# Optimization experiments

Hardware: AMD Instinct MI355X
Metric: run time of the kernel (lower is better)

Reference implementation:

```python
import jax, jax.numpy as jnp
import numpy as np

B, N, E, DIN, DH = 32, 2000, 64000, 128, 128


def setup_inputs() -> dict:
    key = jax.random.key(0)
    ks = jax.random.split(key, 8)
    gene_emb = jax.random.normal(ks[0], (B, N, DIN), dtype=jnp.float32)
    edge_src = jax.random.randint(ks[1], (E,), 0, N, dtype=jnp.int32)
    edge_dst = jax.random.randint(ks[2], (E,), 0, N, dtype=jnp.int32)
    s1 = 1.0 / np.sqrt(DIN)
    s2 = 1.0 / np.sqrt(DH)
    W1 = jax.random.normal(ks[3], (DIN, DH), dtype=jnp.float32) * s1
    b1 = jnp.zeros((DH,), dtype=jnp.float32)
    W2 = jax.random.normal(ks[4], (DH, DH), dtype=jnp.float32) * s2
    b2 = jnp.zeros((DH,), dtype=jnp.float32)
    return {"gene_emb": gene_emb, "edge_src": edge_src, "edge_dst": edge_dst,
            "W1": W1, "b1": b1, "W2": W2, "b2": b2, "pathway_idx": 0}


def _gcn_conv(x, src, dst, norm_e, self_norm, W, b):
    # x: [B, N, Din] -> [B, N, Dout]; PyG GCNConv: linear first, then normalized aggregation
    h = jnp.einsum('bnd,de->bne', x, W)
    msgs = h[:, src, :] * norm_e[None, :, None]          # [B, E, Dout] gather
    agg = jax.vmap(lambda m: jax.ops.segment_sum(m, dst, num_segments=h.shape[1]))(msgs)
    # self-loop contribution (A+I): norm = dinv[i]^2
    return agg + h * self_norm[None, :, None] + b


def reference(gene_emb, edge_src, edge_dst, W1, b1, W2, b2, pathway_idx):
    n = gene_emb.shape[1]
    # symmetric GCN normalization with self loops: deg[i] = in_degree + 1
    deg = jnp.zeros((n,), dtype=gene_emb.dtype).at[edge_dst].add(1.0) + 1.0
    dinv = jax.lax.rsqrt(deg)
    norm_e = dinv[edge_src] * dinv[edge_dst]
    self_norm = dinv * dinv
    x = jax.nn.relu(_gcn_conv(gene_emb, edge_src, edge_dst, norm_e, self_norm, W1, b1))
    x = _gcn_conv(x, edge_src, edge_dst, norm_e, self_norm, W2, b2)
    # global_mean_pool over each graph copy (all graphs have n nodes)
    return jnp.mean(x, axis=1)  # [B, DH]
```

## Files before the change

### kernel.cpp

```cpp
#include <hip/hip_runtime.h>

namespace {
constexpr int NB = 32;
constexpr int NN = 2000;
constexpr int NE = 64000;
constexpr int ND = 128;
constexpr int TR = 32;
constexpr int NCHUNK = (NN + TR - 1) / TR;
constexpr int NXCD = 8;
constexpr int BPB = 2;
constexpr int PAIRS = NB / (NXCD * BPB);
constexpr int GRID_FUSED = NXCD * PAIRS * NCHUNK;
constexpr int SL = 80;
constexpr int ECAP = 1536;

constexpr int CVT_BLOCKS  = 8000;
constexpr int EDGE_BLOCKS = 250;

constexpr size_t OFF_CNT  = 0;
constexpr size_t OFF_WSUM = OFF_CNT + 2048 * 4;
constexpr size_t OFF_SLOT = OFF_WSUM + 2048 * 4;
constexpr size_t OFF_XBF  = OFF_SLOT + (size_t)NN * SL * 4;
constexpr size_t OFF_YP   = OFF_XBF + (size_t)NB * NN * ND * 2;
constexpr size_t MEMSET_BYTES = 2048 * 4 * 2;

__device__ __forceinline__ ushort f32_to_bf16(float f) {
    uint u = __float_as_uint(f);
    u += 0x7fffu + ((u >> 16) & 1u);
    return (ushort)(u >> 16);
}
}

__global__ void k_fill(const float* __restrict__ X, ushort* __restrict__ xbf,
                       const int* __restrict__ src, const int* __restrict__ dst,
                       int* __restrict__ cnt, int* __restrict__ slot) {
    const int blk = blockIdx.x;
    if (blk < CVT_BLOCKS) {
        int i = blk * 256 + threadIdx.x;
        float4 v = ((const float4*)X)[i];
        ushort4 o;
        o.x = f32_to_bf16(v.x);
        o.y = f32_to_bf16(v.y);
        o.z = f32_to_bf16(v.z);
        o.w = f32_to_bf16(v.w);
        ((ushort4*)xbf)[i] = o;
    } else {
        int e = (blk - CVT_BLOCKS) * 256 + threadIdx.x;
        int s = src[e], d = dst[e];
        int p = atomicAdd(&cnt[d], 1);
        if (p < SL) slot[d * SL + p] = s;
    }
}

__global__ void k_wsum(const int* __restrict__ src, const int* __restrict__ dst,
                       const int* __restrict__ cnt, float* __restrict__ wsum) {
    int e = blockIdx.x * 256 + threadIdx.x;
    if (e < NE) {
        int s = src[e], d = dst[e];
        float w = rsqrtf((float)(cnt[s] + 1)) * rsqrtf((float)(cnt[d] + 1));
        atomicAdd(&wsum[s], w);
    }
}

__global__ __launch_bounds__(256, 3) void k_fused(const ushort* __restrict__ xbf,
                                                  const int* __restrict__ cnt,
                                                  const int* __restrict__ slot,
                                                  const float* __restrict__ wsum,
                                                  const float* __restrict__ W1,
                                                  const float* __restrict__ b1,
                                                  float* __restrict__ ypart) {
    __shared__ float4 As4[2][32 * 33];
    __shared__ int2   sEdge[ECAP];
    __shared__ int    sCnt[32];
    __shared__ int    sBase[33];
    __shared__ float  sDinv[32];
    __shared__ float  yred[2][128];
    const int tid = threadIdx.x;

    const int L     = blockIdx.x;
    const int xcd   = L & (NXCD - 1);
    const int sl    = L >> 3;
    const int pair  = sl / NCHUNK;
    const int chunk = sl % NCHUNK;
    const int b0    = xcd * (BPB * PAIRS) + pair * BPB;
    const int n0    = chunk * TR;

    if (tid < 32) {
        int n = n0 + tid;
        int cr = (n < NN) ? cnt[n] : 0;
        sCnt[tid]  = min(cr, SL);
        sDinv[tid] = rsqrtf((float)(cr + 1));
    }
    if (tid < 128) { yred[0][tid] = 0.f; yred[1][tid] = 0.f; }
    __syncthreads();
    if (tid == 0) {
        int s = 0;
        for (int j = 0; j < 32; j++) { sBase[j] = s; s += sCnt[j]; }
        sBase[32] = s;
    }
    __syncthreads();
    const bool staged = (sBase[32] <= ECAP);

    const int wv = tid >> 6, ln = tid & 63;
    if (staged) {
        for (int ii = 0; ii < 8; ii++) {
            int j = wv * 8 + ii;
            int c = sCnt[j];
            float dd = sDinv[j];
            const int* sp = &slot[(size_t)(n0 + j) * SL];
            for (int base = 0; base < c; base += 64) {
                if (base + ln < c) {
                    int sidx = sp[base + ln];
                    float w = rsqrtf((float)(cnt[sidx] + 1)) * dd;
                    sEdge[sBase[j] + base + ln] = make_int2(sidx, __float_as_int(w));
                }
            }
        }
    }
    __syncthreads();

    const uint* __restrict__ Xu0 = (const uint*)(xbf + (size_t)b0 * NN * ND);
    const uint* __restrict__ Xu1 = (const uint*)(xbf + (size_t)(b0 + 1) * NN * ND);
    float2* A0 = (float2*)As4[0];
    float2* A1 = (float2*)As4[1];
    #pragma unroll 1
    for (int ii = 0; ii < 8; ii++) {
        const int j = wv * 8 + ii;
        const int n = n0 + j;
        float2 a0 = make_float2(0.f, 0.f), a1 = a0, a0b = a0, a1b = a0;
        if (n < NN) {
            float sn = sDinv[j]; sn *= sn;
            uint u0 = Xu0[n * 64 + ln], u1 = Xu1[n * 64 + ln];
            a0.x = sn * __uint_as_float(u0 << 16);
            a0.y = sn * __uint_as_float(u0 & 0xffff0000u);
            a1.x = sn * __uint_as_float(u1 << 16);
            a1.y = sn * __uint_as_float(u1 & 0xffff0000u);
            const int c = sCnt[j];
            if (staged) {
                const int e0 = sBase[j], e1 = e0 + c;
                int e = e0;
                for (; e + 8 <= e1; e += 8) {
                    int sidx[8]; float w[8]; uint q0[8], q1[8];
                    #pragma unroll
                    for (int q = 0; q < 8; q++) {
                        int2 ed = sEdge[e + q];
                        sidx[q] = ed.x; w[q] = __int_as_float(ed.y);
                    }
                    #pragma unroll
                    for (int q = 0; q < 8; q++) {
                        q0[q] = Xu0[sidx[q] * 64 + ln];
                        q1[q] = Xu1[sidx[q] * 64 + ln];
                    }
                    #pragma unroll
                    for (int q = 0; q < 8; q++) {
                        float x0l = __uint_as_float(q0[q] << 16);
                        float x0h = __uint_as_float(q0[q] & 0xffff0000u);
                        float x1l = __uint_as_float(q1[q] << 16);
                        float x1h = __uint_as_float(q1[q] & 0xffff0000u);
                        if (q & 1) {
                            a0b.x = fmaf(w[q], x0l, a0b.x);
                            a0b.y = fmaf(w[q], x0h, a0b.y);
                            a1b.x = fmaf(w[q], x1l, a1b.x);
                            a1b.y = fmaf(w[q], x1h, a1b.y);
                        } else {
                            a0.x = fmaf(w[q], x0l, a0.x);
                            a0.y = fmaf(w[q], x0h, a0.y);
                            a1.x = fmaf(w[q], x1l, a1.x);
                            a1.y = fmaf(w[q], x1h, a1.y);
                        }
                    }
                }
                for (; e < e1; e++) {
                    int2 ed = sEdge[e];
                    float w = __int_as_float(ed.y);
                    uint u0e = Xu0[ed.x * 64 + ln], u1e = Xu1[ed.x * 64 + ln];
                    a0.x = fmaf(w, __uint_as_float(u0e << 16), a0.x);
                    a0.y = fmaf(w, __uint_as_float(u0e & 0xffff0000u), a0.y);
                    a1.x = fmaf(w, __uint_as_float(u1e << 16), a1.x);
                    a1.y = fmaf(w, __uint_as_float(u1e & 0xffff0000u), a1.y);
                }
            } else {
                const int* sp = &slot[(size_t)n * SL];
                float dd = sDinv[j];
                for (int e = 0; e < c; e++) {
                    int sidx = sp[e];
                    float w = rsqrtf((float)(cnt[sidx] + 1)) * dd;
                    uint u0e = Xu0[sidx * 64 + ln], u1e = Xu1[sidx * 64 + ln];
                    a0.x = fmaf(w, __uint_as_float(u0e << 16), a0.x);
                    a0.y = fmaf(w, __uint_as_float(u0e & 0xffff0000u), a0.y);
                    a1.x = fmaf(w, __uint_as_float(u1e << 16), a1.x);
                    a1.y = fmaf(w, __uint_as_float(u1e & 0xffff0000u), a1.y);
                }
            }
            a0.x += a0b.x; a0.y += a0b.y;
            a1.x += a1b.x; a1.y += a1b.y;
        }
        A0[j * 66 + ln] = a0;
        A1[j * 66 + ln] = a1;
    }
    __syncthreads();

    const int c4 = tid & 31, rg = tid >> 5;
    float4 acc0[4], acc1[4];
    #pragma unroll
    for (int i = 0; i < 4; i++) {
        acc0[i] = make_float4(0.f, 0.f, 0.f, 0.f);
        acc1[i] = make_float4(0.f, 0.f, 0.f, 0.f);
    }
    const float4* __restrict__ W4 = (const float4*)W1 + c4;
    #pragma unroll 2
    for (int k4 = 0; k4 < 32; k4++) {
        float4 w0 = W4[(4 * k4 + 0) * 32];
        float4 w1 = W4[(4 * k4 + 1) * 32];
        float4 w2 = W4[(4 * k4 + 2) * 32];
        float4 w3 = W4[(4 * k4 + 3) * 32];
        #pragma unroll
        for (int i = 0; i < 4; i++) {
            float4 a = As4[0][(rg * 4 + i) * 33 + k4];
            acc0[i].x = fmaf(a.x, w0.x, acc0[i].x); acc0[i].x = fmaf(a.y, w1.x, acc0[i].x);
            acc0[i].x = fmaf(a.z, w2.x, acc0[i].x); acc0[i].x = fmaf(a.w, w3.x, acc0[i].x);
            acc0[i].y = fmaf(a.x, w0.y, acc0[i].y); acc0[i].y = fmaf(a.y, w1.y, acc0[i].y);
            acc0[i].y = fmaf(a.z, w2.y, acc0[i].y); acc0[i].y = fmaf(a.w, w3.y, acc0[i].y);
            acc0[i].z = fmaf(a.x, w0.z, acc0[i].z); acc0[i].z = fmaf(a.y, w1.z, acc0[i].z);
            acc0[i].z = fmaf(a.z, w2.z, acc0[i].z); acc0[i].z = fmaf(a.w, w3.z, acc0[i].z);
            acc0[i].w = fmaf(a.x, w0.w, acc0[i].w); acc0[i].w = fmaf(a.y, w1.w, acc0[i].w);
            acc0[i].w = fmaf(a.z, w2.w, acc0[i].w); acc0[i].w = fmaf(a.w, w3.w, acc0[i].w);
            float4 b = As4[1][(rg * 4 + i) * 33 + k4];
            acc1[i].x = fmaf(b.x, w0.x, acc1[i].x); acc1[i].x = fmaf(b.y, w1.x, acc1[i].x);
            acc1[i].x = fmaf(b.z, w2.x, acc1[i].x); acc1[i].x = fmaf(b.w, w3.x, acc1[i].x);
            acc1[i].y = fmaf(b.x, w0.y, acc1[i].y); acc1[i].y = fmaf(b.y, w1.y, acc1[i].y);
            acc1[i].y = fmaf(b.z, w2.y, acc1[i].y); acc1[i].y = fmaf(b.w, w3.y, acc1[i].y);
            acc1[i].z = fmaf(b.x, w0.z, acc1[i].z); acc1[i].z = fmaf(b.y, w1.z, acc1[i].z);
            acc1[i].z = fmaf(b.z, w2.z, acc1[i].z); acc1[i].z = fmaf(b.w, w3.z, acc1[i].z);
            acc1[i].w = fmaf(b.x, w0.w, acc1[i].w); acc1[i].w = fmaf(b.y, w1.w, acc1[i].w);
            acc1[i].w = fmaf(b.z, w2.w, acc1[i].w); acc1[i].w = fmaf(b.w, w3.w, acc1[i].w);
        }
    }

    float wn[4];
    #pragma unroll
    for (int i = 0; i < 4; i++) {
        int j = rg * 4 + i, n = n0 + j;
        float sd = sDinv[j];
        wn[i] = (n < NN) ? (wsum[n] + sd * sd) : 0.f;
    }
    float4 bias = ((const float4*)b1)[c4];
    float4 ya0 = make_float4(0.f, 0.f, 0.f, 0.f);
    float4 ya1 = ya0;
    #pragma unroll
    for (int i = 0; i < 4; i++) {
        ya0.x = fmaf(wn[i], fmaxf(acc0[i].x + bias.x, 0.f), ya0.x);
        ya0.y = fmaf(wn[i], fmaxf(acc0[i].y + bias.y, 0.f), ya0.y);
        ya0.z = fmaf(wn[i], fmaxf(acc0[i].z + bias.z, 0.f), ya0.z);
        ya0.w = fmaf(wn[i], fmaxf(acc0[i].w + bias.w, 0.f), ya0.w);
        ya1.x = fmaf(wn[i], fmaxf(acc1[i].x + bias.x, 0.f), ya1.x);
        ya1.y = fmaf(wn[i], fmaxf(acc1[i].y + bias.y, 0.f), ya1.y);
        ya1.z = fmaf(wn[i], fmaxf(acc1[i].z + bias.z, 0.f), ya1.z);
        ya1.w = fmaf(wn[i], fmaxf(acc1[i].w + bias.w, 0.f), ya1.w);
    }
    atomicAdd(&yred[0][4 * c4 + 0], ya0.x); atomicAdd(&yred[0][4 * c4 + 1], ya0.y);
    atomicAdd(&yred[0][4 * c4 + 2], ya0.z); atomicAdd(&yred[0][4 * c4 + 3], ya0.w);
    atomicAdd(&yred[1][4 * c4 + 0], ya1.x); atomicAdd(&yred[1][4 * c4 + 1], ya1.y);
    atomicAdd(&yred[1][4 * c4 + 2], ya1.z); atomicAdd(&yred[1][4 * c4 + 3], ya1.w);
    __syncthreads();
    if (tid < 128)
        ypart[((size_t)b0 * NCHUNK + chunk) * ND + tid] = yred[0][tid];
    else
        ypart[((size_t)(b0 + 1) * NCHUNK + chunk) * ND + (tid - 128)] = yred[1][tid - 128];
}

__global__ __launch_bounds__(128) void k_out(const float* __restrict__ ypart,
                                             const float* __restrict__ W2,
                                             const float* __restrict__ b2,
                                             float* __restrict__ out) {
    __shared__ float ys[128];
    const int b = blockIdx.x;
    const int d = threadIdx.x;
    float s = 0.f;
    for (int c = 0; c < NCHUNK; c++)
        s += ypart[((size_t)b * NCHUNK + c) * ND + d];
    ys[d] = s * (1.f / (float)NN);
    __syncthreads();
    float acc = b2[d];
    #pragma unroll 8
    for (int k = 0; k < 128; k++)
        acc = fmaf(ys[k], W2[k * ND + d], acc);
    out[b * ND + d] = acc;
}

extern "C" void kernel_launch(void* const* d_in, const int* in_sizes, int n_in,
                              void* d_out, int out_size, void* d_ws, size_t ws_size,
                              hipStream_t stream) {
    (void)in_sizes; (void)n_in; (void)out_size; (void)ws_size;
    const float* X   = (const float*)d_in[0];
    const int*   src = (const int*)d_in[1];
    const int*   dst = (const int*)d_in[2];
    const float* W1  = (const float*)d_in[3];
    const float* b1  = (const float*)d_in[4];
    const float* W2  = (const float*)d_in[5];
    const float* b2  = (const float*)d_in[6];
    float* out = (float*)d_out;

    char* ws = (char*)d_ws;
    int*    cnt   = (int*)   (ws + OFF_CNT);
    float*  wsum  = (float*) (ws + OFF_WSUM);
    int*    slot  = (int*)   (ws + OFF_SLOT);
    ushort* xbf   = (ushort*)(ws + OFF_XBF);
    float*  ypart = (float*) (ws + OFF_YP);

    (void)hipMemsetAsync(ws, 0, MEMSET_BYTES, stream);
    k_fill<<<CVT_BLOCKS + EDGE_BLOCKS, 256, 0, stream>>>(X, xbf, src, dst, cnt, slot);
    k_wsum<<<EDGE_BLOCKS, 256, 0, stream>>>(src, dst, cnt, wsum);
    k_fused<<<GRID_FUSED, 256, 0, stream>>>(xbf, cnt, slot, wsum, W1, b1, ypart);
    k_out<<<NB, 128, 0, stream>>>(ypart, W2, b2, out);
}
```

Measured before the change: 195.8 us.

## Use bf16 MFMA for the first-layer transform with prepacked W1 fragments

Replaces the fp32 scalar-FMA 32x128x128 GEMM in the fused kernel with bf16 MFMA 16x16x32 instructions. The aggregated rows are stored to LDS as packed bf16, and W1 is pre-converted into per-lane MFMA fragment layout in an extra section of the fill kernel. Shared memory shrinks and launch bounds rise to 4 blocks per CU, aiming to cut ALU time and raise occupancy. The cost is extra precision loss from rounding the aggregated activations and weights to bf16.

```diff
diff --git a/kernel.cpp b/kernel.cpp
--- a/kernel.cpp
+++ b/kernel.cpp
@@ -15,23 +15,32 @@
 constexpr int ECAP = 1536;
 
 constexpr int CVT_BLOCKS  = 8000;
+constexpr int W_BLOCKS    = 8;
 constexpr int EDGE_BLOCKS = 250;
 
 constexpr size_t OFF_CNT  = 0;
 constexpr size_t OFF_WSUM = OFF_CNT + 2048 * 4;
 constexpr size_t OFF_SLOT = OFF_WSUM + 2048 * 4;
-constexpr size_t OFF_XBF  = OFF_SLOT + (size_t)NN * SL * 4;
+constexpr size_t OFF_WF   = OFF_SLOT + (size_t)NN * SL * 4;
+constexpr size_t OFF_XBF  = OFF_WF + 32768;
 constexpr size_t OFF_YP   = OFF_XBF + (size_t)NB * NN * ND * 2;
 constexpr size_t MEMSET_BYTES = 2048 * 4 * 2;
+
+typedef __attribute__((ext_vector_type(8))) short bf16x8;
+typedef __attribute__((ext_vector_type(4))) float f32x4;
 
 __device__ __forceinline__ ushort f32_to_bf16(float f) {
     uint u = __float_as_uint(f);
     u += 0x7fffu + ((u >> 16) & 1u);
     return (ushort)(u >> 16);
 }
+__device__ __forceinline__ uint pack_bf16x2(float lo, float hi) {
+    return (uint)f32_to_bf16(lo) | ((uint)f32_to_bf16(hi) << 16);
+}
 }
 
 __global__ void k_fill(const float* __restrict__ X, ushort* __restrict__ xbf,
+                       const float* __restrict__ W1, uint* __restrict__ wf,
                        const int* __restrict__ src, const int* __restrict__ dst,
                        int* __restrict__ cnt, int* __restrict__ slot) {
     const int blk = blockIdx.x;
@@ -44,8 +53,20 @@
         o.z = f32_to_bf16(v.z);
         o.w = f32_to_bf16(v.w);
         ((ushort4*)xbf)[i] = o;
+    } else if (blk < CVT_BLOCKS + W_BLOCKS) {
+        int g = (blk - CVT_BLOCKS) * 256 + threadIdx.x;
+        int lane = g & 63, f = g >> 6;
+        int nt = f >> 2, kc = f & 3;
+        int col = nt * 16 + (lane & 15);
+        int k0  = kc * 32 + (lane >> 4) * 8;
+        uint4 o;
+        o.x = pack_bf16x2(W1[(k0 + 0) * ND + col], W1[(k0 + 1) * ND + col]);
+        o.y = pack_bf16x2(W1[(k0 + 2) * ND + col], W1[(k0 + 3) * ND + col]);
+        o.z = pack_bf16x2(W1[(k0 + 4) * ND + col], W1[(k0 + 5) * ND + col]);
+        o.w = pack_bf16x2(W1[(k0 + 6) * ND + col], W1[(k0 + 7) * ND + col]);
+        ((uint4*)wf)[g] = o;
     } else {
-        int e = (blk - CVT_BLOCKS) * 256 + threadIdx.x;
+        int e = (blk - CVT_BLOCKS - W_BLOCKS) * 256 + threadIdx.x;
         int s = src[e], d = dst[e];
         int p = atomicAdd(&cnt[d], 1);
         if (p < SL) slot[d * SL + p] = s;
@@ -62,19 +83,20 @@
     }
 }
 
-__global__ __launch_bounds__(256, 3) void k_fused(const ushort* __restrict__ xbf,
+__global__ __launch_bounds__(256, 4) void k_fused(const ushort* __restrict__ xbf,
                                                   const int* __restrict__ cnt,
                                                   const int* __restrict__ slot,
                                                   const float* __restrict__ wsum,
-                                                  const float* __restrict__ W1,
+                                                  const uint* __restrict__ wfrag,
                                                   const float* __restrict__ b1,
                                                   float* __restrict__ ypart) {
-    __shared__ float4 As4[2][32 * 33];
-    __shared__ int2   sEdge[ECAP];
-    __shared__ int    sCnt[32];
-    __shared__ int    sBase[33];
-    __shared__ float  sDinv[32];
-    __shared__ float  yred[2][128];
+    __shared__ uint  AsU[2][32 * 68];
+    __shared__ int2  sEdge[ECAP];
+    __shared__ int   sCnt[32];
+    __shared__ int   sBase[33];
+    __shared__ float sDinv[32];
+    __shared__ float sWn[32];
+    __shared__ float yred[2][128];
     const int tid = threadIdx.x;
 
     const int L     = blockIdx.x;
@@ -88,8 +110,10 @@
     if (tid < 32) {
         int n = n0 + tid;
         int cr = (n < NN) ? cnt[n] : 0;
+        float d = rsqrtf((float)(cr + 1));
         sCnt[tid]  = min(cr, SL);
-        sDinv[tid] = rsqrtf((float)(cr + 1));
+        sDinv[tid] = d;
+        sWn[tid]   = (n < NN) ? (wsum[n] + d * d) : 0.f;
     }
     if (tid < 128) { yred[0][tid] = 0.f; yred[1][tid] = 0.f; }
     __syncthreads();
@@ -121,8 +145,6 @@
 
     const uint* __restrict__ Xu0 = (const uint*)(xbf + (size_t)b0 * NN * ND);
     const uint* __restrict__ Xu1 = (const uint*)(xbf + (size_t)(b0 + 1) * NN * ND);
-    float2* A0 = (float2*)As4[0];
-    float2* A1 = (float2*)As4[1];
     #pragma unroll 1
     for (int ii = 0; ii < 8; ii++) {
         const int j = wv * 8 + ii;
@@ -195,73 +217,67 @@
             a0.x += a0b.x; a0.y += a0b.y;
             a1.x += a1b.x; a1.y += a1b.y;
         }
-        A0[j * 66 + ln] = a0;
-        A1[j * 66 + ln] = a1;
-    }
-    __syncthreads();
-
-    const int c4 = tid & 31, rg = tid >> 5;
-    float4 acc0[4], acc1[4];
+        AsU[0][j * 68 + ln] = pack_bf16x2(a0.x, a0.y);
+        AsU[1][j * 68 + ln] = pack_bf16x2(a1.x, a1.y);
+    }
+    __syncthreads();
+
+    const int lane15 = ln & 15, quad = ln >> 4;
+    f32x4 zero4 = {0.f, 0.f, 0.f, 0.f};
+    f32x4 acc[2][2][2];
     #pragma unroll
-    for (int i = 0; i < 4; i++) {
-        acc0[i] = make_float4(0.f, 0.f, 0.f, 0.f);
-        acc1[i] = make_float4(0.f, 0.f, 0.f, 0.f);
-    }
-    const float4* __restrict__ W4 = (const float4*)W1 + c4;
-    #pragma unroll 2
-    for (int k4 = 0; k4 < 32; k4++) {
-        float4 w0 = W4[(4 * k4 + 0) * 32];
-        float4 w1 = W4[(4 * k4 + 1) * 32];
-        float4 w2 = W4[(4 * k4 + 2) * 32];
-        float4 w3 = W4[(4 * k4 + 3) * 32];
+    for (int b = 0; b < 2; b++)
         #pragma unroll
-        for (int i = 0; i < 4; i++) {
-            float4 a = As4[0][(rg * 4 + i) * 33 + k4];
-            acc0[i].x = fmaf(a.x, w0.x, acc0[i].x); acc0[i].x = fmaf(a.y, w1.x, acc0[i].x);
-            acc0[i].x = fmaf(a.z, w2.x, acc0[i].x); acc0[i].x = fmaf(a.w, w3.x, acc0[i].x);
-            acc0[i].y = fmaf(a.x, w0.y, acc0[i].y); acc0[i].y = fmaf(a.y, w1.y, acc0[i].y);
-            acc0[i].y = fmaf(a.z, w2.y, acc0[i].y); acc0[i].y = fmaf(a.w, w3.y, acc0[i].y);
-            acc0[i].z = fmaf(a.x, w0.z, acc0[i].z); acc0[i].z = fmaf(a.y, w1.z, acc0[i].z);
-            acc0[i].z = fmaf(a.z, w2.z, acc0[i].z); acc0[i].z = fmaf(a.w, w3.z, acc0[i].z);
-            acc0[i].w = fmaf(a.x, w0.w, acc0[i].w); acc0[i].w = fmaf(a.y, w1.w, acc0[i].w);
-            acc0[i].w = fmaf(a.z, w2.w, acc0[i].w); acc0[i].w = fmaf(a.w, w3.w, acc0[i].w);
-            float4 b = As4[1][(rg * 4 + i) * 33 + k4];
-            acc1[i].x = fmaf(b.x, w0.x, acc1[i].x); acc1[i].x = fmaf(b.y, w1.x, acc1[i].x);
-            acc1[i].x = fmaf(b.z, w2.x, acc1[i].x); acc1[i].x = fmaf(b.w, w3.x, acc1[i].x);
-            acc1[i].y = fmaf(b.x, w0.y, acc1[i].y); acc1[i].y = fmaf(b.y, w1.y, acc1[i].y);
-            acc1[i].y = fmaf(b.z, w2.y, acc1[i].y); acc1[i].y = fmaf(b.w, w3.y, acc1[i].y);
-            acc1[i].z = fmaf(b.x, w0.z, acc1[i].z); acc1[i].z = fmaf(b.y, w1.z, acc1[i].z);
-            acc1[i].z = fmaf(b.z, w2.z, acc1[i].z); acc1[i].z = fmaf(b.w, w3.z, acc1[i].z);
-            acc1[i].w = fmaf(b.x, w0.w, acc1[i].w); acc1[i].w = fmaf(b.y, w1.w, acc1[i].w);
-            acc1[i].w = fmaf(b.z, w2.w, acc1[i].w); acc1[i].w = fmaf(b.w, w3.w, acc1[i].w);
+        for (int mt = 0; mt < 2; mt++)
+            #pragma unroll
+            for (int nt2 = 0; nt2 < 2; nt2++) acc[b][mt][nt2] = zero4;
+
+    bf16x8 wf[2][4];
+    const bf16x8* Wf8 = (const bf16x8*)wfrag;
+    #pragma unroll
+    for (int nt2 = 0; nt2 < 2; nt2++)
+        #pragma unroll
+        for (int kc = 0; kc < 4; kc++)
+            wf[nt2][kc] = Wf8[(((2 * wv + nt2) * 4 + kc) * 64) + ln];
+
+    const bf16x8* A8_0 = (const bf16x8*)AsU[0];
+    const bf16x8* A8_1 = (const bf16x8*)AsU[1];
+    #pragma unroll
+    for (int mt = 0; mt < 2; mt++) {
+        const int r = mt * 16 + lane15;
+        #pragma unroll
+        for (int kc = 0; kc < 4; kc++) {
+            bf16x8 af0 = A8_0[r * 17 + kc * 4 + quad];
+            bf16x8 af1 = A8_1[r * 17 + kc * 4 + quad];
+            #pragma unroll
+            for (int nt2 = 0; nt2 < 2; nt2++) {
+                acc[0][mt][nt2] = __builtin_amdgcn_mfma_f32_16x16x32_bf16(
+                    af0, wf[nt2][kc], acc[0][mt][nt2], 0, 0, 0);
+                acc[1][mt][nt2] = __builtin_amdgcn_mfma_f32_16x16x32_bf16(
+                    af1, wf[nt2][kc], acc[1][mt][nt2], 0, 0, 0);
+            }
         }
     }
 
-    float wn[4];
     #pragma unroll
-    for (int i = 0; i < 4; i++) {
-        int j = rg * 4 + i, n = n0 + j;
-        float sd = sDinv[j];
-        wn[i] = (n < NN) ? (wsum[n] + sd * sd) : 0.f;
-    }
-    float4 bias = ((const float4*)b1)[c4];
-    float4 ya0 = make_float4(0.f, 0.f, 0.f, 0.f);
-    float4 ya1 = ya0;
-    #pragma unroll
-    for (int i = 0; i < 4; i++) {
-        ya0.x = fmaf(wn[i], fmaxf(acc0[i].x + bias.x, 0.f), ya0.x);
-        ya0.y = fmaf(wn[i], fmaxf(acc0[i].y + bias.y, 0.f), ya0.y);
-        ya0.z = fmaf(wn[i], fmaxf(acc0[i].z + bias.z, 0.f), ya0.z);
-        ya0.w = fmaf(wn[i], fmaxf(acc0[i].w + bias.w, 0.f), ya0.w);
-        ya1.x = fmaf(wn[i], fmaxf(acc1[i].x + bias.x, 0.f), ya1.x);
-        ya1.y = fmaf(wn[i], fmaxf(acc1[i].y + bias.y, 0.f), ya1.y);
-        ya1.z = fmaf(wn[i], fmaxf(acc1[i].z + bias.z, 0.f), ya1.z);
-        ya1.w = fmaf(wn[i], fmaxf(acc1[i].w + bias.w, 0.f), ya1.w);
-    }
-    atomicAdd(&yred[0][4 * c4 + 0], ya0.x); atomicAdd(&yred[0][4 * c4 + 1], ya0.y);
-    atomicAdd(&yred[0][4 * c4 + 2], ya0.z); atomicAdd(&yred[0][4 * c4 + 3], ya0.w);
-    atomicAdd(&yred[1][4 * c4 + 0], ya1.x); atomicAdd(&yred[1][4 * c4 + 1], ya1.y);
-    atomicAdd(&yred[1][4 * c4 + 2], ya1.z); atomicAdd(&yred[1][4 * c4 + 3], ya1.w);
+    for (int nt2 = 0; nt2 < 2; nt2++) {
+        int cg = (2 * wv + nt2) * 16 + lane15;
+        float bias = b1[cg];
+        #pragma unroll
+        for (int b = 0; b < 2; b++) {
+            float part = 0.f;
+            #pragma unroll
+            for (int mt = 0; mt < 2; mt++) {
+                f32x4 a = acc[b][mt][nt2];
+                #pragma unroll
+                for (int r = 0; r < 4; r++) {
+                    int m = mt * 16 + quad * 4 + r;
+                    part = fmaf(sWn[m], fmaxf(a[r] + bias, 0.f), part);
+                }
+            }
+            atomicAdd(&yred[b][cg], part);
+        }
+    }
     __syncthreads();
     if (tid < 128)
         ypart[((size_t)b0 * NCHUNK + chunk) * ND + tid] = yred[0][tid];
@@ -305,12 +321,14 @@
     int*    cnt   = (int*)   (ws + OFF_CNT);
     float*  wsum  = (float*) (ws + OFF_WSUM);
     int*    slot  = (int*)   (ws + OFF_SLOT);
+    uint*   wfb   = (uint*)  (ws + OFF_WF);
     ushort* xbf   = (ushort*)(ws + OFF_XBF);
     float*  ypart = (float*) (ws + OFF_YP);
 
     (void)hipMemsetAsync(ws, 0, MEMSET_BYTES, stream);
-    k_fill<<<CVT_BLOCKS + EDGE_BLOCKS, 256, 0, stream>>>(X, xbf, src, dst, cnt, slot);
+    k_fill<<<CVT_BLOCKS + W_BLOCKS + EDGE_BLOCKS, 256, 0, stream>>>(
+        X, xbf, W1, wfb, src, dst, cnt, slot);
     k_wsum<<<EDGE_BLOCKS, 256, 0, stream>>>(src, dst, cnt, wsum);
-    k_fused<<<GRID_FUSED, 256, 0, stream>>>(xbf, cnt, slot, wsum, W1, b1, ypart);
+    k_fused<<<GRID_FUSED, 256, 0, stream>>>(xbf, cnt, slot, wsum, wfb, b1, ypart);
     k_out<<<NB, 128, 0, stream>>>(ypart, W2, b2, out);
 }
```

Result: faster. 164.6 us (-16.0%).
